# Performance work log

Measured on AMD Instinct MI355X. Metric: run time of the kernel, lower is better.

The kernel has to match this reference:

```python
import jax, jax.numpy as jnp
import numpy as np

B, H, W, D = 16, 14, 14, 512   # map_dim D == attention_dim A (required by broadcast add)
L, HID, A = 32, 512, 512


def setup_inputs() -> dict:
    key = jax.random.key(0)
    ks = jax.random.split(key, 8)
    s = 0.02
    return {
        "maps": jax.random.normal(ks[0], (B, H, W, D), jnp.float32),
        "hiddens": jax.random.normal(ks[1], (B, L, HID), jnp.float32),
        "W_hidden": jax.random.normal(ks[2], (A, HID), jnp.float32) * s,
        "b_hidden": jnp.zeros((A,), jnp.float32),
        "W_rect": jax.random.normal(ks[3], (1, A), jnp.float32) * s,
        "b_rect": jnp.zeros((1,), jnp.float32),
        "W_co": jax.random.normal(ks[4], (HID, D), jnp.float32) * s,
        "b_co": jnp.zeros((HID,), jnp.float32),
    }


def reference(maps, hiddens, W_hidden, b_hidden, W_rect, b_rect, W_co, b_co):
    b, h, w, d = maps.shape
    fmaps = maps.reshape(b, h * w, d)                       # (B, P, D)
    hlin = hiddens @ W_hidden.T + b_hidden                  # (B, L, A)
    # additive co-attention score: ReLU(fmaps + hlin) -> linear to scalar
    rect = jax.nn.relu(fmaps[:, None, :, :] + hlin[:, :, None, :])  # (B, L, P, A)
    scores = jnp.einsum('blpa,a->blp', rect, W_rect[0]) + b_rect[0]  # (B, L, P)
    attn = jax.nn.softmax(scores, axis=2)                   # softmax over pixels P
    ctx = jnp.einsum('blp,bpd->bld', attn, fmaps)           # (B, L, D)
    co_att = (ctx @ W_co.T + b_co) * hiddens                # (B, L, HID)
    return co_att, attn
```

## Files before the change

### kernel.cpp

```cpp
#include <hip/hip_runtime.h>
#include <math.h>


typedef __attribute__((ext_vector_type(8))) short short8;
typedef __attribute__((ext_vector_type(4))) float f32x4;

__device__ __forceinline__ unsigned f2bf_u(float x) {
    union { float f; unsigned u; } c; c.f = x;
    return (c.u + 0x7FFFu + ((c.u >> 16) & 1u)) >> 16;
}
__device__ __forceinline__ unsigned pack2(float lo, float hi) {
    return f2bf_u(lo) | (f2bf_u(hi) << 16);
}
__device__ __forceinline__ uint4 pack8(const float4 a, const float4 b) {
    uint4 r;
    r.x = pack2(a.x, a.y); r.y = pack2(a.z, a.w);
    r.z = pack2(b.x, b.y); r.w = pack2(b.z, b.w);
    return r;
}

template<int HMUL>
__global__ __launch_bounds__(256) void gemm_kernel(
    const float* __restrict__ Af, const float* __restrict__ Bf,
    const float* __restrict__ bias, const float* __restrict__ hmul,
    float* __restrict__ C)
{
    __shared__ __align__(16) char smem[65536];
    uint4* As = (uint4*)smem;
    uint4* Bs = (uint4*)(smem + 32768);
    float* red = (float*)smem;
    const int tid = threadIdx.x, bid = blockIdx.x;

    const int m0 = (bid >> 4) * 32, n0 = (bid & 15) * 32;
    #pragma unroll
    for (int j = 0; j < 8; ++j) {
        const int S = tid + 256 * j;
        const int i = S >> 6, ln = S & 63;
        const int t = i & 1, s = i >> 1;
        const int row  = t * 16 + (ln & 15);
        const int col8 = s * 4 + (ln >> 4);
        const float* ap = Af + (size_t)(m0 + row) * 512 + col8 * 8;
        const float* bp = Bf + (size_t)(n0 + row) * 512 + col8 * 8;
        As[S] = pack8(*(const float4*)ap, *(const float4*)(ap + 4));
        Bs[S] = pack8(*(const float4*)bp, *(const float4*)(bp + 4));
    }
    __syncthreads();

    const int w = tid >> 6, ln = tid & 63;
    f32x4 acc[4];
    #pragma unroll
    for (int fo = 0; fo < 4; ++fo) acc[fo] = (f32x4){0.f,0.f,0.f,0.f};
    #pragma unroll
    for (int sl = 0; sl < 4; ++sl) {
        const int s = 4 * w + sl;
        const short8 a0 = *(const short8*)&As[(2*s+0)*64 + ln];
        const short8 a1 = *(const short8*)&As[(2*s+1)*64 + ln];
        const short8 b0 = *(const short8*)&Bs[(2*s+0)*64 + ln];
        const short8 b1 = *(const short8*)&Bs[(2*s+1)*64 + ln];
        acc[0] = __builtin_amdgcn_mfma_f32_16x16x32_bf16(a0, b0, acc[0], 0, 0, 0);
        acc[1] = __builtin_amdgcn_mfma_f32_16x16x32_bf16(a0, b1, acc[1], 0, 0, 0);
        acc[2] = __builtin_amdgcn_mfma_f32_16x16x32_bf16(a1, b0, acc[2], 0, 0, 0);
        acc[3] = __builtin_amdgcn_mfma_f32_16x16x32_bf16(a1, b1, acc[3], 0, 0, 0);
    }
    __syncthreads();
    #pragma unroll
    for (int fo = 0; fo < 4; ++fo)
        #pragma unroll
        for (int r = 0; r < 4; ++r)
            red[w*1024 + fo*256 + r*64 + ln] = acc[fo][r];
    __syncthreads();
    #pragma unroll
    for (int j = 0; j < 4; ++j) {
        const int o = tid + 256 * j;
        float v = red[o] + red[1024 + o] + red[2048 + o] + red[3072 + o];
        const int fo = o >> 8, r = (o >> 6) & 3, l2 = o & 63;
        const int m = m0 + (fo >> 1) * 16 + ((l2 >> 4) << 2) + r;
        const int n = n0 + (fo & 1) * 16 + (l2 & 15);
        v += bias[n];
        if (HMUL) v *= hmul[(size_t)m * 512 + n];
        C[(size_t)m * 512 + n] = v;
    }
}

__global__ __launch_bounds__(256) void mid_kernel(
    const float* __restrict__ maps, const float* __restrict__ hlin,
    const float* __restrict__ W_rect, const float* __restrict__ b_rect,
    float* __restrict__ attn_out, float* __restrict__ ctx_out)
{
    const int b = blockIdx.x >> 4, s = blockIdx.x & 15;
    const int l0 = 2 * s;
    const int tid = threadIdx.x;
    const int pi = tid >> 4, k = tid & 15;

    __shared__ float h0[512], h1[512], wv[512];
    __shared__ float ftile[16 * 516];
    __shared__ float red0[208 * 16], red1[208 * 16];
    __shared__ float sm[2 * 208];

    {
        const float4* H0 = (const float4*)(hlin + ((size_t)b * 32 + l0) * 512);
        const float4* H1 = (const float4*)(hlin + ((size_t)b * 32 + l0 + 1) * 512);
        const float4* WV = (const float4*)W_rect;
        if (tid < 128) { ((float4*)h0)[tid] = H0[tid]; ((float4*)wv)[tid] = WV[tid]; }
        else           { ((float4*)h1)[tid - 128] = H1[tid - 128]; }
    }
    __syncthreads();

    int aoff[8];
    float4 h0r[8], h1r[8], wr[8];
    #pragma unroll
    for (int j = 0; j < 8; ++j) {
        aoff[j] = k * 32 + ((j + k) & 7) * 4;
        h0r[j] = *(const float4*)&h0[aoff[j]];
        h1r[j] = *(const float4*)&h1[aoff[j]];
        wr[j]  = *(const float4*)&wv[aoff[j]];
    }

    const float* mb = maps + (size_t)b * 196 * 512;

    for (int c = 0; c < 13; ++c) {
        __syncthreads();
        #pragma unroll
        for (int it = 0; it < 8; ++it) {
            const int idx = tid + 256 * it;
            const int r = idx >> 7, c4 = idx & 127;
            int p = c * 16 + r; if (p > 195) p = 195;
            *(float4*)&ftile[r * 516 + c4 * 4] = *(const float4*)(mb + (size_t)p * 512 + c4 * 4);
        }
        __syncthreads();
        float s0 = 0.f, s1 = 0.f;
        #pragma unroll
        for (int j = 0; j < 8; ++j) {
            const float4 f = *(const float4*)&ftile[pi * 516 + aoff[j]];
            const float4 A = h0r[j], Bv = h1r[j], W = wr[j];
            s0 += fmaxf(f.x + A.x, 0.f) * W.x + fmaxf(f.y + A.y, 0.f) * W.y
                + fmaxf(f.z + A.z, 0.f) * W.z + fmaxf(f.w + A.w, 0.f) * W.w;
            s1 += fmaxf(f.x + Bv.x, 0.f) * W.x + fmaxf(f.y + Bv.y, 0.f) * W.y
                + fmaxf(f.z + Bv.z, 0.f) * W.z + fmaxf(f.w + Bv.w, 0.f) * W.w;
        }
        const int p = c * 16 + pi;
        red0[p * 16 + k] = s0;
        red1[p * 16 + k] = s1;
    }
    __syncthreads();

    const float br = b_rect[0];
    for (int idx = tid; idx < 392; idx += 256) {
        const int l = idx & 1, p = idx >> 1;
        const float* rb = (l ? red1 : red0) + p * 16;
        const float4 a = *(const float4*)rb,      bq = *(const float4*)(rb + 4);
        const float4 cq = *(const float4*)(rb + 8), dq = *(const float4*)(rb + 12);
        sm[l * 208 + p] = (a.x + a.y + a.z + a.w) + (bq.x + bq.y + bq.z + bq.w)
                        + (cq.x + cq.y + cq.z + cq.w) + (dq.x + dq.y + dq.z + dq.w) + br;
    }
    __syncthreads();

    const int wave = tid >> 6, lane = tid & 63;
    if (wave < 2) {
        float v[4];
        #pragma unroll
        for (int i = 0; i < 4; ++i) {
            const int p = lane + 64 * i;
            v[i] = (p < 196) ? sm[wave * 208 + p] : -INFINITY;
        }
        float m = fmaxf(fmaxf(v[0], v[1]), fmaxf(v[2], v[3]));
        for (int off = 32; off > 0; off >>= 1) m = fmaxf(m, __shfl_down(m, off));
        m = __shfl(m, 0);
        float e[4], ssum = 0.f;
        #pragma unroll
        for (int i = 0; i < 4; ++i) {
            const int p = lane + 64 * i;
            e[i] = (p < 196) ? __expf(v[i] - m) : 0.f;
            ssum += e[i];
        }
        for (int off = 32; off > 0; off >>= 1) ssum += __shfl_down(ssum, off);
        ssum = __shfl(ssum, 0);
        const float inv = 1.f / ssum;
        float* ao = attn_out + ((size_t)b * 32 + l0 + wave) * 196;
        #pragma unroll
        for (int i = 0; i < 4; ++i) {
            const int p = lane + 64 * i;
            if (p < 196) {
                const float at = e[i] * inv;
                sm[wave * 208 + p] = at;
                ao[p] = at;
            }
        }
    }
    __syncthreads();

    const int d0 = tid * 2;
    float a0 = 0.f, a1 = 0.f, c0 = 0.f, c1 = 0.f;
    for (int p = 0; p < 196; ++p) {
        const float2 f = *(const float2*)(mb + (size_t)p * 512 + d0);
        const float w0 = sm[p], w1 = sm[208 + p];
        a0 += w0 * f.x; a1 += w0 * f.y;
        c0 += w1 * f.x; c1 += w1 * f.y;
    }
    float2 o0; o0.x = a0; o0.y = a1;
    float2 o1; o1.x = c0; o1.y = c1;
    *(float2*)(ctx_out + ((size_t)b * 32 + l0) * 512 + d0)     = o0;
    *(float2*)(ctx_out + ((size_t)b * 32 + l0 + 1) * 512 + d0) = o1;
}

extern "C" void kernel_launch(void* const* d_in, const int* in_sizes, int n_in,
                              void* d_out, int out_size, void* d_ws, size_t ws_size,
                              hipStream_t stream)
{
    const float* maps     = (const float*)d_in[0];
    const float* hiddens  = (const float*)d_in[1];
    const float* W_hidden = (const float*)d_in[2];
    const float* b_hidden = (const float*)d_in[3];
    const float* W_rect   = (const float*)d_in[4];
    const float* b_rect   = (const float*)d_in[5];
    const float* W_co     = (const float*)d_in[6];
    const float* b_co     = (const float*)d_in[7];

    float* out_co   = (float*)d_out;
    float* out_attn = out_co + (size_t)512 * 512;
    float* ctx      = (float*)d_ws;

    hipLaunchKernelGGL((gemm_kernel<0>), dim3(256), dim3(256), 0, stream,
                       hiddens, W_hidden, b_hidden, (const float*)nullptr, out_co);
    hipLaunchKernelGGL(mid_kernel, dim3(256), dim3(256), 0, stream,
                       maps, out_co, W_rect, b_rect, out_attn, ctx);
    hipLaunchKernelGGL((gemm_kernel<1>), dim3(256), dim3(256), 0, stream,
                       ctx, W_co, b_co, hiddens, out_co);
}
```

Before: 106.0 us.

## Fuse online softmax and context accumulation into score loop; bf16 ctx; pipeline GEMM loads

The mid kernel now runs an online softmax per 16-pixel chunk and accumulates the context from the shared-memory tile already loaded. This removes the second full pass over maps from global memory and the large per-pixel reduction buffers. The context is written as bf16, which halves its traffic and lets the second GEMM skip the float-to-bf16 packing. The GEMM splits K into two halves and issues the second half's global loads before the first half's MFMAs to overlap them. In exchange, the mid kernel adds three extra barriers per chunk and serial reductions on 32 threads, and the bf16 context adds rounding error.

```diff
diff --git a/kernel.cpp b/kernel.cpp
--- a/kernel.cpp
+++ b/kernel.cpp
@@ -19,50 +19,94 @@
     return r;
 }
 
-template<int HMUL>
+template<int MODE>
 __global__ __launch_bounds__(256) void gemm_kernel(
-    const float* __restrict__ Af, const float* __restrict__ Bf,
-    const float* __restrict__ bias, const float* __restrict__ hmul,
-    float* __restrict__ C)
+    const float* __restrict__ Af, const unsigned short* __restrict__ Ab,
+    const float* __restrict__ Bf, const float* __restrict__ bias,
+    const float* __restrict__ hmul, float* __restrict__ C)
 {
-    __shared__ __align__(16) char smem[65536];
-    uint4* As = (uint4*)smem;
-    uint4* Bs = (uint4*)(smem + 32768);
-    float* red = (float*)smem;
+    __shared__ uint4 As[2][1024];
+    __shared__ uint4 Bs[2][1024];
     const int tid = threadIdx.x, bid = blockIdx.x;
-
     const int m0 = (bid >> 4) * 32, n0 = (bid & 15) * 32;
-    #pragma unroll
-    for (int j = 0; j < 8; ++j) {
+
+    #pragma unroll
+    for (int j = 0; j < 4; ++j) {
         const int S = tid + 256 * j;
         const int i = S >> 6, ln = S & 63;
-        const int t = i & 1, s = i >> 1;
-        const int row  = t * 16 + (ln & 15);
-        const int col8 = s * 4 + (ln >> 4);
-        const float* ap = Af + (size_t)(m0 + row) * 512 + col8 * 8;
+        const int row = (i & 1) * 16 + (ln & 15);
+        const int col8 = (i >> 1) * 4 + (ln >> 4);
+        uint4 av;
+        if (MODE == 0) {
+            const float* ap = Af + (size_t)(m0 + row) * 512 + col8 * 8;
+            av = pack8(*(const float4*)ap, *(const float4*)(ap + 4));
+        } else {
+            av = *(const uint4*)(Ab + (size_t)(m0 + row) * 512 + col8 * 8);
+        }
         const float* bp = Bf + (size_t)(n0 + row) * 512 + col8 * 8;
-        As[S] = pack8(*(const float4*)ap, *(const float4*)(ap + 4));
-        Bs[S] = pack8(*(const float4*)bp, *(const float4*)(bp + 4));
-    }
-    __syncthreads();
+        As[0][S] = av;
+        Bs[0][S] = pack8(*(const float4*)bp, *(const float4*)(bp + 4));
+    }
+    __syncthreads();
+
+    float4 raf[4][2], rbf[4][2]; uint4 rab[4];
+    #pragma unroll
+    for (int j = 0; j < 4; ++j) {
+        const int S = tid + 256 * j;
+        const int i = S >> 6, ln = S & 63;
+        const int row = (i & 1) * 16 + (ln & 15);
+        const int col8 = (8 + (i >> 1)) * 4 + (ln >> 4);
+        if (MODE == 0) {
+            const float* ap = Af + (size_t)(m0 + row) * 512 + col8 * 8;
+            raf[j][0] = *(const float4*)ap; raf[j][1] = *(const float4*)(ap + 4);
+        } else {
+            rab[j] = *(const uint4*)(Ab + (size_t)(m0 + row) * 512 + col8 * 8);
+        }
+        const float* bp = Bf + (size_t)(n0 + row) * 512 + col8 * 8;
+        rbf[j][0] = *(const float4*)bp; rbf[j][1] = *(const float4*)(bp + 4);
+    }
 
     const int w = tid >> 6, ln = tid & 63;
     f32x4 acc[4];
     #pragma unroll
     for (int fo = 0; fo < 4; ++fo) acc[fo] = (f32x4){0.f,0.f,0.f,0.f};
-    #pragma unroll
-    for (int sl = 0; sl < 4; ++sl) {
-        const int s = 4 * w + sl;
-        const short8 a0 = *(const short8*)&As[(2*s+0)*64 + ln];
-        const short8 a1 = *(const short8*)&As[(2*s+1)*64 + ln];
-        const short8 b0 = *(const short8*)&Bs[(2*s+0)*64 + ln];
-        const short8 b1 = *(const short8*)&Bs[(2*s+1)*64 + ln];
+
+    #pragma unroll
+    for (int sl = 0; sl < 2; ++sl) {
+        const int s_loc = (w + 4 * sl);
+        const short8 a0 = *(const short8*)&As[0][(2*s_loc+0)*64 + ln];
+        const short8 a1 = *(const short8*)&As[0][(2*s_loc+1)*64 + ln];
+        const short8 b0 = *(const short8*)&Bs[0][(2*s_loc+0)*64 + ln];
+        const short8 b1 = *(const short8*)&Bs[0][(2*s_loc+1)*64 + ln];
         acc[0] = __builtin_amdgcn_mfma_f32_16x16x32_bf16(a0, b0, acc[0], 0, 0, 0);
         acc[1] = __builtin_amdgcn_mfma_f32_16x16x32_bf16(a0, b1, acc[1], 0, 0, 0);
         acc[2] = __builtin_amdgcn_mfma_f32_16x16x32_bf16(a1, b0, acc[2], 0, 0, 0);
         acc[3] = __builtin_amdgcn_mfma_f32_16x16x32_bf16(a1, b1, acc[3], 0, 0, 0);
     }
-    __syncthreads();
+
+    #pragma unroll
+    for (int j = 0; j < 4; ++j) {
+        const int S = tid + 256 * j;
+        As[1][S] = (MODE == 0) ? pack8(raf[j][0], raf[j][1]) : rab[j];
+        Bs[1][S] = pack8(rbf[j][0], rbf[j][1]);
+    }
+    __syncthreads();
+
+    #pragma unroll
+    for (int sl = 0; sl < 2; ++sl) {
+        const int s_loc = (w + 4 * sl);
+        const short8 a0 = *(const short8*)&As[1][(2*s_loc+0)*64 + ln];
+        const short8 a1 = *(const short8*)&As[1][(2*s_loc+1)*64 + ln];
+        const short8 b0 = *(const short8*)&Bs[1][(2*s_loc+0)*64 + ln];
+        const short8 b1 = *(const short8*)&Bs[1][(2*s_loc+1)*64 + ln];
+        acc[0] = __builtin_amdgcn_mfma_f32_16x16x32_bf16(a0, b0, acc[0], 0, 0, 0);
+        acc[1] = __builtin_amdgcn_mfma_f32_16x16x32_bf16(a0, b1, acc[1], 0, 0, 0);
+        acc[2] = __builtin_amdgcn_mfma_f32_16x16x32_bf16(a1, b0, acc[2], 0, 0, 0);
+        acc[3] = __builtin_amdgcn_mfma_f32_16x16x32_bf16(a1, b1, acc[3], 0, 0, 0);
+    }
+    __syncthreads();
+
+    float* red = (float*)&As[0][0];
     #pragma unroll
     for (int fo = 0; fo < 4; ++fo)
         #pragma unroll
@@ -77,7 +121,7 @@
         const int m = m0 + (fo >> 1) * 16 + ((l2 >> 4) << 2) + r;
         const int n = n0 + (fo & 1) * 16 + (l2 & 15);
         v += bias[n];
-        if (HMUL) v *= hmul[(size_t)m * 512 + n];
+        if (MODE == 1) v *= hmul[(size_t)m * 512 + n];
         C[(size_t)m * 512 + n] = v;
     }
 }
@@ -85,7 +129,7 @@
 __global__ __launch_bounds__(256) void mid_kernel(
     const float* __restrict__ maps, const float* __restrict__ hlin,
     const float* __restrict__ W_rect, const float* __restrict__ b_rect,
-    float* __restrict__ attn_out, float* __restrict__ ctx_out)
+    float* __restrict__ attn_out, unsigned int* __restrict__ ctx_out)
 {
     const int b = blockIdx.x >> 4, s = blockIdx.x & 15;
     const int l0 = 2 * s;
@@ -94,8 +138,10 @@
 
     __shared__ float h0[512], h1[512], wv[512];
     __shared__ float ftile[16 * 516];
-    __shared__ float red0[208 * 16], red1[208 * 16];
-    __shared__ float sm[2 * 208];
+    __shared__ float part0[16 * 16], part1[16 * 16];
+    __shared__ float sraw[2 * 208];
+    __shared__ float ep[2 * 16];
+    __shared__ float bc[4];
 
     {
         const float4* H0 = (const float4*)(hlin + ((size_t)b * 32 + l0) * 512);
@@ -117,6 +163,11 @@
     }
 
     const float* mb = maps + (size_t)b * 196 * 512;
+    const float br = b_rect[0];
+    const int d0 = tid * 2;
+
+    float m0 = -INFINITY, m1 = -INFINITY, ls0 = 0.f, ls1 = 0.f;
+    float cA0 = 0.f, cA1 = 0.f, cB0 = 0.f, cB1 = 0.f;
 
     for (int c = 0; c < 13; ++c) {
         __syncthreads();
@@ -128,6 +179,7 @@
             *(float4*)&ftile[r * 516 + c4 * 4] = *(const float4*)(mb + (size_t)p * 512 + c4 * 4);
         }
         __syncthreads();
+
         float s0 = 0.f, s1 = 0.f;
         #pragma unroll
         for (int j = 0; j < 8; ++j) {
@@ -138,69 +190,64 @@
             s1 += fmaxf(f.x + Bv.x, 0.f) * W.x + fmaxf(f.y + Bv.y, 0.f) * W.y
                 + fmaxf(f.z + Bv.z, 0.f) * W.z + fmaxf(f.w + Bv.w, 0.f) * W.w;
         }
-        const int p = c * 16 + pi;
-        red0[p * 16 + k] = s0;
-        red1[p * 16 + k] = s1;
-    }
-    __syncthreads();
-
-    const float br = b_rect[0];
+        part0[pi * 16 + k] = s0;
+        part1[pi * 16 + k] = s1;
+        __syncthreads();
+
+        if (tid < 32) {
+            const int l = tid >> 4, pl = tid & 15;
+            const float* pb = (l ? part1 : part0) + pl * 16;
+            const float4 q0 = *(const float4*)pb,       q1 = *(const float4*)(pb + 4);
+            const float4 q2 = *(const float4*)(pb + 8), q3 = *(const float4*)(pb + 12);
+            float sc = (q0.x+q0.y+q0.z+q0.w) + (q1.x+q1.y+q1.z+q1.w)
+                     + (q2.x+q2.y+q2.z+q2.w) + (q3.x+q3.y+q3.z+q3.w) + br;
+            const int p = c * 16 + pl;
+            if (p > 195) sc = -INFINITY;
+            sraw[l * 208 + p] = sc;
+            float mx = sc;
+            #pragma unroll
+            for (int msk = 1; msk <= 8; msk <<= 1) mx = fmaxf(mx, __shfl_xor(mx, msk));
+            if (pl == 0) bc[l] = mx;
+        }
+        __syncthreads();
+
+        const float nm0 = fmaxf(m0, bc[0]), nm1 = fmaxf(m1, bc[1]);
+        if (tid < 32) {
+            const int l = tid >> 4, pl = tid & 15;
+            const int p = c * 16 + pl;
+            const float sc = sraw[l * 208 + p];
+            const float e = (p > 195) ? 0.f : __expf(sc - (l ? nm1 : nm0));
+            ep[l * 16 + pl] = e;
+            float es = e;
+            #pragma unroll
+            for (int msk = 1; msk <= 8; msk <<= 1) es += __shfl_xor(es, msk);
+            if (pl == 0) bc[2 + l] = es;
+        }
+        __syncthreads();
+
+        const float al0 = __expf(m0 - nm0), al1 = __expf(m1 - nm1);
+        ls0 = ls0 * al0 + bc[2];
+        ls1 = ls1 * al1 + bc[3];
+        m0 = nm0; m1 = nm1;
+        cA0 *= al0; cA1 *= al0; cB0 *= al1; cB1 *= al1;
+        #pragma unroll
+        for (int r = 0; r < 16; ++r) {
+            const float2 f = *(const float2*)&ftile[r * 516 + d0];
+            const float w0 = ep[r], w1 = ep[16 + r];
+            cA0 += w0 * f.x; cA1 += w0 * f.y;
+            cB0 += w1 * f.x; cB1 += w1 * f.y;
+        }
+    }
+
+    const float inv0 = 1.f / ls0, inv1 = 1.f / ls1;
+    ctx_out[((size_t)b * 32 + l0) * 256 + tid]     = pack2(cA0 * inv0, cA1 * inv0);
+    ctx_out[((size_t)b * 32 + l0 + 1) * 256 + tid] = pack2(cB0 * inv1, cB1 * inv1);
     for (int idx = tid; idx < 392; idx += 256) {
         const int l = idx & 1, p = idx >> 1;
-        const float* rb = (l ? red1 : red0) + p * 16;
-        const float4 a = *(const float4*)rb,      bq = *(const float4*)(rb + 4);
-        const float4 cq = *(const float4*)(rb + 8), dq = *(const float4*)(rb + 12);
-        sm[l * 208 + p] = (a.x + a.y + a.z + a.w) + (bq.x + bq.y + bq.z + bq.w)
-                        + (cq.x + cq.y + cq.z + cq.w) + (dq.x + dq.y + dq.z + dq.w) + br;
-    }
-    __syncthreads();
-
-    const int wave = tid >> 6, lane = tid & 63;
-    if (wave < 2) {
-        float v[4];
-        #pragma unroll
-        for (int i = 0; i < 4; ++i) {
-            const int p = lane + 64 * i;
-            v[i] = (p < 196) ? sm[wave * 208 + p] : -INFINITY;
-        }
-        float m = fmaxf(fmaxf(v[0], v[1]), fmaxf(v[2], v[3]));
-        for (int off = 32; off > 0; off >>= 1) m = fmaxf(m, __shfl_down(m, off));
-        m = __shfl(m, 0);
-        float e[4], ssum = 0.f;
-        #pragma unroll
-        for (int i = 0; i < 4; ++i) {
-            const int p = lane + 64 * i;
-            e[i] = (p < 196) ? __expf(v[i] - m) : 0.f;
-            ssum += e[i];
-        }
-        for (int off = 32; off > 0; off >>= 1) ssum += __shfl_down(ssum, off);
-        ssum = __shfl(ssum, 0);
-        const float inv = 1.f / ssum;
-        float* ao = attn_out + ((size_t)b * 32 + l0 + wave) * 196;
-        #pragma unroll
-        for (int i = 0; i < 4; ++i) {
-            const int p = lane + 64 * i;
-            if (p < 196) {
-                const float at = e[i] * inv;
-                sm[wave * 208 + p] = at;
-                ao[p] = at;
-            }
-        }
-    }
-    __syncthreads();
-
-    const int d0 = tid * 2;
-    float a0 = 0.f, a1 = 0.f, c0 = 0.f, c1 = 0.f;
-    for (int p = 0; p < 196; ++p) {
-        const float2 f = *(const float2*)(mb + (size_t)p * 512 + d0);
-        const float w0 = sm[p], w1 = sm[208 + p];
-        a0 += w0 * f.x; a1 += w0 * f.y;
-        c0 += w1 * f.x; c1 += w1 * f.y;
-    }
-    float2 o0; o0.x = a0; o0.y = a1;
-    float2 o1; o1.x = c0; o1.y = c1;
-    *(float2*)(ctx_out + ((size_t)b * 32 + l0) * 512 + d0)     = o0;
-    *(float2*)(ctx_out + ((size_t)b * 32 + l0 + 1) * 512 + d0) = o1;
+        const float sc = sraw[l * 208 + p];
+        attn_out[((size_t)b * 32 + l0 + l) * 196 + p] =
+            __expf(sc - (l ? m1 : m0)) * (l ? inv1 : inv0);
+    }
 }
 
 extern "C" void kernel_launch(void* const* d_in, const int* in_sizes, int n_in,
@@ -218,12 +265,14 @@
 
     float* out_co   = (float*)d_out;
     float* out_attn = out_co + (size_t)512 * 512;
-    float* ctx      = (float*)d_ws;
+    unsigned int*   ctx32 = (unsigned int*)d_ws;
+    unsigned short* ctx16 = (unsigned short*)d_ws;
 
     hipLaunchKernelGGL((gemm_kernel<0>), dim3(256), dim3(256), 0, stream,
-                       hiddens, W_hidden, b_hidden, (const float*)nullptr, out_co);
+                       hiddens, (const unsigned short*)nullptr, W_hidden, b_hidden,
+                       (const float*)nullptr, out_co);
     hipLaunchKernelGGL(mid_kernel, dim3(256), dim3(256), 0, stream,
-                       maps, out_co, W_rect, b_rect, out_attn, ctx);
+                       maps, out_co, W_rect, b_rect, out_attn, ctx32);
     hipLaunchKernelGGL((gemm_kernel<1>), dim3(256), dim3(256), 0, stream,
-                       ctx, W_co, b_co, hiddens, out_co);
-}
+                       (const float*)nullptr, ctx16, W_co, b_co, hiddens, out_co);
+}
```

After: 108.2 us. 2.0% more time.
